# Optimization experiments

Hardware: AMD Instinct MI355X
Metric: run time of the kernel (lower is better)

The kernel has to match this reference:

```python
import jax, jax.numpy as jnp
import numpy as np
from jax import lax

BN_EPS = 1e-5

def dwconv(x, w, dilation):
    # x: [N,C,H,W], w: [C,1,k,k] depthwise; SAME padding = (r*(k-1)+1)//2
    k = w.shape[-1]
    pad = (dilation * (k - 1) + 1) // 2
    return lax.conv_general_dilated(
        x, w, window_strides=(1, 1), padding=[(pad, pad), (pad, pad)],
        rhs_dilation=(dilation, dilation), feature_group_count=x.shape[1],
        dimension_numbers=('NCHW', 'OIHW', 'NCHW'))

def bn_eval(y, gamma, beta, mean, var):
    # inference BatchNorm2d over channel dim; params: [C]
    inv = gamma * lax.rsqrt(var + BN_EPS)
    return y * inv[None, :, None, None] + (beta - mean * inv)[None, :, None, None]

def setup_inputs() -> dict:
    key = jax.random.key(0)
    ks = jax.random.split(key, 13)
    C = 384
    x = jax.random.normal(ks[0], (16, C, 56, 56), jnp.float32)
    w_lk = jax.random.normal(ks[1], (C, 1, 13, 13), jnp.float32) * 0.05
    w_b0 = jax.random.normal(ks[2], (C, 1, 5, 5), jnp.float32) * 0.05
    w_b1 = jax.random.normal(ks[3], (C, 1, 7, 7), jnp.float32) * 0.05
    w_b2 = jax.random.normal(ks[4], (C, 1, 7, 7), jnp.float32) * 0.05
    w_b3 = jax.random.normal(ks[5], (C, 1, 3, 3), jnp.float32) * 0.05
    w_b4 = jax.random.normal(ks[6], (C, 1, 3, 3), jnp.float32) * 0.05
    w_b5 = jax.random.normal(ks[7], (C, 1, 3, 3), jnp.float32) * 0.05
    bn_gamma = jax.random.uniform(ks[8], (7, C), jnp.float32, 0.5, 1.5)
    bn_beta = jax.random.normal(ks[9], (7, C), jnp.float32) * 0.1
    bn_mean = jax.random.normal(ks[10], (7, C), jnp.float32) * 0.1
    bn_var = jax.random.uniform(ks[11], (7, C), jnp.float32, 0.5, 1.5)
    return dict(x=x, w_lk=w_lk, w_b0=w_b0, w_b1=w_b1, w_b2=w_b2, w_b3=w_b3,
                w_b4=w_b4, w_b5=w_b5, bn_gamma=bn_gamma, bn_beta=bn_beta,
                bn_mean=bn_mean, bn_var=bn_var)

def reference(x, w_lk, w_b0, w_b1, w_b2, w_b3, w_b4, w_b5,
              bn_gamma, bn_beta, bn_mean, bn_var):
    # DilatedReparamBlock (kernel_size=13, non-deploy):
    # out = BN(dw13(x)) + sum_i BN_i(dw_{k_i, r_i}(x))
    dilates = (1, 1, 2, 3, 4, 5)
    branch_ws = (w_b0, w_b1, w_b2, w_b3, w_b4, w_b5)
    out = bn_eval(dwconv(x, w_lk, 1), bn_gamma[0], bn_beta[0], bn_mean[0], bn_var[0])
    for i, (w, r) in enumerate(zip(branch_ws, dilates)):
        j = i + 1
        out = out + bn_eval(dwconv(x, w, r), bn_gamma[j], bn_beta[j], bn_mean[j], bn_var[j])
    return out
```

## Files before the change

kernel.cpp:

```cpp
#include <hip/hip_runtime.h>


#define CCH 384
#define SP 56
#define PW 68
#define NPLANES (16*384)

__global__ __launch_bounds__(64) void drb_conv13_w64(
    const float* __restrict__ x,
    const float* __restrict__ w_lk, const float* __restrict__ w_b0,
    const float* __restrict__ w_b1, const float* __restrict__ w_b2,
    const float* __restrict__ w_b3, const float* __restrict__ w_b4,
    const float* __restrict__ w_b5,
    const float* __restrict__ gamma, const float* __restrict__ beta,
    const float* __restrict__ mean, const float* __restrict__ var,
    float* __restrict__ out)
{
    __shared__ __align__(16) float sx[PW * PW];
    __shared__ __align__(16) float sw[13 * 16];

    const int plane = blockIdx.x;
    const int c = plane % CCH;
    const int tid = threadIdx.x;
    const float* __restrict__ xp = x + (size_t)plane * (SP * SP);

    float S[7];
    float bias = 0.f;
    #pragma unroll
    for (int j = 0; j < 7; j++) {
        float inv = gamma[j * CCH + c] * rsqrtf(var[j * CCH + c] + 1e-5f);
        S[j] = inv;
        bias += beta[j * CCH + c] - mean[j * CCH + c] * inv;
    }

    {
        float4 z = make_float4(0.f, 0.f, 0.f, 0.f);
        #pragma unroll
        for (int k = 0; k < 19; k++) {
            int i = tid + 64 * k;
            if (i < PW * PW / 4) ((float4*)sx)[i] = z;
        }
    }

    #pragma unroll
    for (int k = 0; k < 4; k++) {
        int t = tid + 64 * k;
        if (t < 13 * 16) {
            int ky = t >> 4, kx = t & 15;
            float w = 0.f;
            if (kx < 13) {
                w = S[0] * w_lk[c * 169 + ky * 13 + kx];
                if (ky >= 4 && ky <= 8 && kx >= 4 && kx <= 8)
                    w += S[1] * w_b0[c * 25 + (ky - 4) * 5 + (kx - 4)];
                if (ky >= 3 && ky <= 9 && kx >= 3 && kx <= 9)
                    w += S[2] * w_b1[c * 49 + (ky - 3) * 7 + (kx - 3)];
                if (!(ky & 1) && !(kx & 1))
                    w += S[3] * w_b2[c * 49 + (ky >> 1) * 7 + (kx >> 1)];
                if (ky >= 3 && ky <= 9 && (ky - 3) % 3 == 0 &&
                    kx >= 3 && kx <= 9 && (kx - 3) % 3 == 0)
                    w += S[4] * w_b3[c * 9 + ((ky - 3) / 3) * 3 + (kx - 3) / 3];
                if (ky >= 2 && ky <= 10 && (ky - 2) % 4 == 0 &&
                    kx >= 2 && kx <= 10 && (kx - 2) % 4 == 0)
                    w += S[5] * w_b4[c * 9 + ((ky - 2) / 4) * 3 + (kx - 2) / 4];
                if (ky >= 1 && ky <= 11 && (ky - 1) % 5 == 0 &&
                    kx >= 1 && kx <= 11 && (kx - 1) % 5 == 0)
                    w += S[6] * w_b5[c * 9 + ((ky - 1) / 5) * 3 + (kx - 1) / 5];
            }
            sw[t] = w;
        }
    }

    #pragma unroll
    for (int k = 0; k < 13; k++) {
        int i4 = tid + 64 * k;
        if (i4 < SP * SP / 4) {
            float4 v = ((const float4*)xp)[i4];
            int r = i4 / 14;
            int col = (i4 - r * 14) * 4;
            float* d = &sx[(r + 6) * PW + col + 6];
            ((float2*)d)[0] = make_float2(v.x, v.y);
            ((float2*)d)[1] = make_float2(v.z, v.w);
        }
    }
    __syncthreads();

    const int xg = tid & 7;
    const int yg = tid >> 3;
    const int xgc = (xg < 7) ? xg : 3;
    const int Yb = yg * 7;
    const float* __restrict__ sbase = &sx[Yb * PW + 8 * xgc];

    float acc[7][8];
    #pragma unroll
    for (int r = 0; r < 7; r++)
        #pragma unroll
        for (int j = 0; j < 8; j++) acc[r][j] = 0.f;

    #pragma unroll 1
    for (int k0 = 0; k0 < 12; k0 += 2) {
        float4 w0[4], w1[4];
        #pragma unroll
        for (int q = 0; q < 4; q++) {
            w0[q] = ((const float4*)&sw[k0 * 16])[q];
            w1[q] = ((const float4*)&sw[(k0 + 1) * 16])[q];
        }
        const float* sr = sbase + k0 * PW;
        #pragma unroll
        for (int i = 0; i < 8; i++) {
            float4 win4[5];
            #pragma unroll
            for (int q = 0; q < 5; q++)
                win4[q] = *(const float4*)(sr + i * PW + 4 * q);
            const float* win = (const float*)win4;
            if (i < 7) {
                #pragma unroll
                for (int kx = 0; kx < 13; kx++) {
                    const float wv = ((const float*)w0)[kx];
                    #pragma unroll
                    for (int j = 0; j < 8; j++)
                        acc[i][j] = fmaf(wv, win[kx + j], acc[i][j]);
                }
            }
            if (i >= 1) {
                #pragma unroll
                for (int kx = 0; kx < 13; kx++) {
                    const float wv = ((const float*)w1)[kx];
                    #pragma unroll
                    for (int j = 0; j < 8; j++)
                        acc[i - 1][j] = fmaf(wv, win[kx + j], acc[i - 1][j]);
                }
            }
        }
    }
    {
        float4 wt[4];
        #pragma unroll
        for (int q = 0; q < 4; q++) wt[q] = ((const float4*)&sw[12 * 16])[q];
        const float* sr = sbase + 12 * PW;
        #pragma unroll
        for (int i = 0; i < 7; i++) {
            float4 win4[5];
            #pragma unroll
            for (int q = 0; q < 5; q++)
                win4[q] = *(const float4*)(sr + i * PW + 4 * q);
            const float* win = (const float*)win4;
            #pragma unroll
            for (int kx = 0; kx < 13; kx++) {
                const float wv = ((const float*)wt)[kx];
                #pragma unroll
                for (int j = 0; j < 8; j++)
                    acc[i][j] = fmaf(wv, win[kx + j], acc[i][j]);
            }
        }
    }

    if (xg < 7) {
        float* op = out + (size_t)plane * (SP * SP) + Yb * SP + 8 * xg;
        #pragma unroll
        for (int r = 0; r < 7; r++) {
            float4 v0 = make_float4(acc[r][0] + bias, acc[r][1] + bias,
                                    acc[r][2] + bias, acc[r][3] + bias);
            float4 v1 = make_float4(acc[r][4] + bias, acc[r][5] + bias,
                                    acc[r][6] + bias, acc[r][7] + bias);
            *(float4*)(op + r * SP) = v0;
            *(float4*)(op + r * SP + 4) = v1;
        }
    }
}

extern "C" void kernel_launch(void* const* d_in, const int* in_sizes, int n_in,
                              void* d_out, int out_size, void* d_ws, size_t ws_size,
                              hipStream_t stream) {
    const float* x    = (const float*)d_in[0];
    const float* w_lk = (const float*)d_in[1];
    const float* w_b0 = (const float*)d_in[2];
    const float* w_b1 = (const float*)d_in[3];
    const float* w_b2 = (const float*)d_in[4];
    const float* w_b3 = (const float*)d_in[5];
    const float* w_b4 = (const float*)d_in[6];
    const float* w_b5 = (const float*)d_in[7];
    const float* bn_g = (const float*)d_in[8];
    const float* bn_b = (const float*)d_in[9];
    const float* bn_m = (const float*)d_in[10];
    const float* bn_v = (const float*)d_in[11];
    float* out = (float*)d_out;

    drb_conv13_w64<<<dim3(NPLANES), dim3(64), 0, stream>>>(
        x, w_lk, w_b0, w_b1, w_b2, w_b3, w_b4, w_b5,
        bn_g, bn_b, bn_m, bn_v, out);
}
```

Before: 245.6 us.

## Split each plane across two waves with narrower 7x4 per-thread tiles

Doubles the block to 128 threads and gives each thread a 7x4 output tile instead of 7x8. 112 of the 128 threads are active, against 56 of 64 before. The merged 13x13 weights are packed densely, and each pass of the vertical loop now covers four kernel rows, so every shared-memory window row feeds up to four accumulator rows. The aim is more in-flight waves per plane and lower register pressure, at the cost of more redundant window loads per output. It also adds a barrier between the shared-memory zeroing and the interior fill.

```diff
diff --git a/kernel.cpp b/kernel.cpp
--- a/kernel.cpp
+++ b/kernel.cpp
@@ -5,8 +5,9 @@
 #define SP 56
 #define PW 68
 #define NPLANES (16*384)
+#define BLK 128
 
-__global__ __launch_bounds__(64) void drb_conv13_w64(
+__global__ __launch_bounds__(BLK, 4) void drb_conv13_2w(
     const float* __restrict__ x,
     const float* __restrict__ w_lk, const float* __restrict__ w_b0,
     const float* __restrict__ w_b1, const float* __restrict__ w_b2,
@@ -17,7 +18,7 @@
     float* __restrict__ out)
 {
     __shared__ __align__(16) float sx[PW * PW];
-    __shared__ __align__(16) float sw[13 * 16];
+    __shared__ __align__(16) float sw[176];
 
     const int plane = blockIdx.x;
     const int c = plane % CCH;
@@ -36,43 +37,41 @@
     {
         float4 z = make_float4(0.f, 0.f, 0.f, 0.f);
         #pragma unroll
-        for (int k = 0; k < 19; k++) {
-            int i = tid + 64 * k;
+        for (int k = 0; k < 10; k++) {
+            int i = tid + BLK * k;
             if (i < PW * PW / 4) ((float4*)sx)[i] = z;
         }
     }
+    __syncthreads();
 
     #pragma unroll
-    for (int k = 0; k < 4; k++) {
-        int t = tid + 64 * k;
-        if (t < 13 * 16) {
-            int ky = t >> 4, kx = t & 15;
-            float w = 0.f;
-            if (kx < 13) {
-                w = S[0] * w_lk[c * 169 + ky * 13 + kx];
-                if (ky >= 4 && ky <= 8 && kx >= 4 && kx <= 8)
-                    w += S[1] * w_b0[c * 25 + (ky - 4) * 5 + (kx - 4)];
-                if (ky >= 3 && ky <= 9 && kx >= 3 && kx <= 9)
-                    w += S[2] * w_b1[c * 49 + (ky - 3) * 7 + (kx - 3)];
-                if (!(ky & 1) && !(kx & 1))
-                    w += S[3] * w_b2[c * 49 + (ky >> 1) * 7 + (kx >> 1)];
-                if (ky >= 3 && ky <= 9 && (ky - 3) % 3 == 0 &&
-                    kx >= 3 && kx <= 9 && (kx - 3) % 3 == 0)
-                    w += S[4] * w_b3[c * 9 + ((ky - 3) / 3) * 3 + (kx - 3) / 3];
-                if (ky >= 2 && ky <= 10 && (ky - 2) % 4 == 0 &&
-                    kx >= 2 && kx <= 10 && (kx - 2) % 4 == 0)
-                    w += S[5] * w_b4[c * 9 + ((ky - 2) / 4) * 3 + (kx - 2) / 4];
-                if (ky >= 1 && ky <= 11 && (ky - 1) % 5 == 0 &&
-                    kx >= 1 && kx <= 11 && (kx - 1) % 5 == 0)
-                    w += S[6] * w_b5[c * 9 + ((ky - 1) / 5) * 3 + (kx - 1) / 5];
-            }
+    for (int k = 0; k < 2; k++) {
+        int t = tid + BLK * k;
+        if (t < 169) {
+            int ky = t / 13, kx = t - 13 * ky;
+            float w = S[0] * w_lk[c * 169 + t];
+            if (ky >= 4 && ky <= 8 && kx >= 4 && kx <= 8)
+                w += S[1] * w_b0[c * 25 + (ky - 4) * 5 + (kx - 4)];
+            if (ky >= 3 && ky <= 9 && kx >= 3 && kx <= 9)
+                w += S[2] * w_b1[c * 49 + (ky - 3) * 7 + (kx - 3)];
+            if (!(ky & 1) && !(kx & 1))
+                w += S[3] * w_b2[c * 49 + (ky >> 1) * 7 + (kx >> 1)];
+            if (ky >= 3 && ky <= 9 && (ky - 3) % 3 == 0 &&
+                kx >= 3 && kx <= 9 && (kx - 3) % 3 == 0)
+                w += S[4] * w_b3[c * 9 + ((ky - 3) / 3) * 3 + (kx - 3) / 3];
+            if (ky >= 2 && ky <= 10 && (ky - 2) % 4 == 0 &&
+                kx >= 2 && kx <= 10 && (kx - 2) % 4 == 0)
+                w += S[5] * w_b4[c * 9 + ((ky - 2) / 4) * 3 + (kx - 2) / 4];
+            if (ky >= 1 && ky <= 11 && (ky - 1) % 5 == 0 &&
+                kx >= 1 && kx <= 11 && (kx - 1) % 5 == 0)
+                w += S[6] * w_b5[c * 9 + ((ky - 1) / 5) * 3 + (kx - 1) / 5];
             sw[t] = w;
         }
     }
 
     #pragma unroll
-    for (int k = 0; k < 13; k++) {
-        int i4 = tid + 64 * k;
+    for (int k = 0; k < 7; k++) {
+        int i4 = tid + BLK * k;
         if (i4 < SP * SP / 4) {
             float4 v = ((const float4*)xp)[i4];
             int r = i4 / 14;
@@ -84,86 +83,80 @@
     }
     __syncthreads();
 
-    const int xg = tid & 7;
-    const int yg = tid >> 3;
-    const int xgc = (xg < 7) ? xg : 3;
+    const int tact = (tid < 112) ? tid : 0;
+    const int xg = tact % 14;
+    const int yg = tact / 14;
     const int Yb = yg * 7;
-    const float* __restrict__ sbase = &sx[Yb * PW + 8 * xgc];
+    const float* __restrict__ sbase = &sx[Yb * PW + 4 * xg];
 
-    float acc[7][8];
+    float acc[7][4];
     #pragma unroll
     for (int r = 0; r < 7; r++)
         #pragma unroll
-        for (int j = 0; j < 8; j++) acc[r][j] = 0.f;
+        for (int j = 0; j < 4; j++) acc[r][j] = 0.f;
 
     #pragma unroll 1
-    for (int k0 = 0; k0 < 12; k0 += 2) {
-        float4 w0[4], w1[4];
+    for (int g = 0; g < 3; g++) {
+        const int k0 = g * 4;
+        float4 wq[13];
         #pragma unroll
-        for (int q = 0; q < 4; q++) {
-            w0[q] = ((const float4*)&sw[k0 * 16])[q];
-            w1[q] = ((const float4*)&sw[(k0 + 1) * 16])[q];
-        }
+        for (int q = 0; q < 13; q++)
+            wq[q] = ((const float4*)&sw[k0 * 13])[q];
+        const float* w = (const float*)wq;
         const float* sr = sbase + k0 * PW;
         #pragma unroll
-        for (int i = 0; i < 8; i++) {
-            float4 win4[5];
+        for (int i = 0; i < 10; i++) {
+            float4 win4[4];
             #pragma unroll
-            for (int q = 0; q < 5; q++)
+            for (int q = 0; q < 4; q++)
                 win4[q] = *(const float4*)(sr + i * PW + 4 * q);
             const float* win = (const float*)win4;
-            if (i < 7) {
-                #pragma unroll
-                for (int kx = 0; kx < 13; kx++) {
-                    const float wv = ((const float*)w0)[kx];
+            #pragma unroll
+            for (int d = 0; d < 4; d++) {
+                const int r = i - d;
+                if (r >= 0 && r <= 6) {
                     #pragma unroll
-                    for (int j = 0; j < 8; j++)
-                        acc[i][j] = fmaf(wv, win[kx + j], acc[i][j]);
-                }
-            }
-            if (i >= 1) {
-                #pragma unroll
-                for (int kx = 0; kx < 13; kx++) {
-                    const float wv = ((const float*)w1)[kx];
-                    #pragma unroll
-                    for (int j = 0; j < 8; j++)
-                        acc[i - 1][j] = fmaf(wv, win[kx + j], acc[i - 1][j]);
+                    for (int kx = 0; kx < 13; kx++) {
+                        const float wv = w[d * 13 + kx];
+                        #pragma unroll
+                        for (int j = 0; j < 4; j++)
+                            acc[r][j] = fmaf(wv, win[kx + j], acc[r][j]);
+                    }
                 }
             }
         }
     }
     {
-        float4 wt[4];
+        float wt[13];
         #pragma unroll
-        for (int q = 0; q < 4; q++) wt[q] = ((const float4*)&sw[12 * 16])[q];
+        for (int q = 0; q < 3; q++)
+            ((float4*)wt)[q] = ((const float4*)&sw[156])[q];
+        wt[12] = sw[168];
         const float* sr = sbase + 12 * PW;
         #pragma unroll
-        for (int i = 0; i < 7; i++) {
-            float4 win4[5];
+        for (int r = 0; r < 7; r++) {
+            float4 win4[4];
             #pragma unroll
-            for (int q = 0; q < 5; q++)
-                win4[q] = *(const float4*)(sr + i * PW + 4 * q);
+            for (int q = 0; q < 4; q++)
+                win4[q] = *(const float4*)(sr + r * PW + 4 * q);
             const float* win = (const float*)win4;
             #pragma unroll
             for (int kx = 0; kx < 13; kx++) {
-                const float wv = ((const float*)wt)[kx];
+                const float wv = wt[kx];
                 #pragma unroll
-                for (int j = 0; j < 8; j++)
-                    acc[i][j] = fmaf(wv, win[kx + j], acc[i][j]);
+                for (int j = 0; j < 4; j++)
+                    acc[r][j] = fmaf(wv, win[kx + j], acc[r][j]);
             }
         }
     }
 
-    if (xg < 7) {
-        float* op = out + (size_t)plane * (SP * SP) + Yb * SP + 8 * xg;
+    if (tid < 112) {
+        float* op = out + (size_t)plane * (SP * SP) + Yb * SP + 4 * xg;
         #pragma unroll
         for (int r = 0; r < 7; r++) {
-            float4 v0 = make_float4(acc[r][0] + bias, acc[r][1] + bias,
-                                    acc[r][2] + bias, acc[r][3] + bias);
-            float4 v1 = make_float4(acc[r][4] + bias, acc[r][5] + bias,
-                                    acc[r][6] + bias, acc[r][7] + bias);
-            *(float4*)(op + r * SP) = v0;
-            *(float4*)(op + r * SP + 4) = v1;
+            float4 v = make_float4(acc[r][0] + bias, acc[r][1] + bias,
+                                   acc[r][2] + bias, acc[r][3] + bias);
+            *(float4*)(op + r * SP) = v;
         }
     }
 }
@@ -185,7 +178,7 @@
     const float* bn_v = (const float*)d_in[11];
     float* out = (float*)d_out;
 
-    drb_conv13_w64<<<dim3(NPLANES), dim3(64), 0, stream>>>(
+    drb_conv13_2w<<<dim3(NPLANES), dim3(BLK), 0, stream>>>(
         x, w_lk, w_b0, w_b1, w_b2, w_b3, w_b4, w_b5,
         bn_g, bn_b, bn_m, bn_v, out);
 }
```

New measurement: 252.7 us. +2.9%, slower.
